# Kernel optimization log

Hardware: AMD Instinct MI355X
Metric: run time of the kernel (lower is better)

## Reference

```python
import jax, jax.numpy as jnp
import numpy as np

N = 8192          # n_nodes; must equal OUT due to _weight_norm broadcasting
IN = 512          # in_features
OUT = 8192        # out_features
ALPHA = 0.2       # leaky relu negative slope
NEG_INF = -9e15   # mask value used by the torch module


def setup_inputs() -> dict:
    key = jax.random.key(0)
    k1, k2, k3, k4 = jax.random.split(key, 4)
    x = jax.random.normal(k1, (N, IN), jnp.float32)
    adj = jax.random.randint(k2, (N, N), 0, 2, jnp.int32)
    # nn.Linear weight [out_features, in_features]
    W = jax.random.normal(k3, (OUT, IN), jnp.float32) / np.sqrt(IN)
    # attention vector a: [2*out_features, 1], xavier_uniform-ish scale
    a = jax.random.normal(k4, (2 * OUT, 1), jnp.float32) * (1.414 * np.sqrt(2.0 / (2 * OUT + 1)))
    return {"x": x, "adj": adj, "W": W, "a": a}


def reference(x, adj, W, a):
    h = x @ W.T                                   # [N, OUT] (OUT == N)
    # torch._weight_norm(h, g, dim=1) = h * g / ||h||_cols  (norm over dim 0, kept as [1, OUT])
    col_norm = jnp.linalg.norm(h, axis=0, keepdims=True)   # [1, OUT]
    a1 = a[:OUT]                                  # [OUT, 1]
    a2 = a[OUT:]                                  # [OUT, 1]
    wn1 = h * (a1 / col_norm)                     # [N, N]: h[i,j]*a1[i]/norm[j]
    wn2 = h * (a2 / col_norm)                     # [N, N]
    e = jax.nn.leaky_relu(wn1 + wn2.T, ALPHA)     # [N, N]
    scores = jnp.where(adj > 0, e, NEG_INF)
    attention = jax.nn.softmax(scores, axis=1)    # dropout omitted (eval / deterministic)
    return attention @ h                          # [N, OUT]
```

## Files before the change

### kernel.cpp

```cpp
#include <hip/hip_runtime.h>
#include <hip/hip_bf16.h>
#include <stdint.h>

#define NN 8192
#define KIN 512

typedef __attribute__((ext_vector_type(8))) short bfx8;
typedef __attribute__((ext_vector_type(4))) float f32x4;
typedef __attribute__((ext_vector_type(4))) short sh4;

__device__ __forceinline__ float b2f(unsigned short u) {
  union { unsigned int i; float f; } z; z.i = ((unsigned int)u) << 16; return z.f;
}
__device__ __forceinline__ unsigned short f2b(float f) {
  __hip_bfloat16 h = __float2bfloat16(f);
  union { __hip_bfloat16 h; unsigned short u; } z; z.h = h; return z.u;
}

__device__ __forceinline__ void async16(void* lds, const void* g) {
  __builtin_amdgcn_global_load_lds(
      (const __attribute__((address_space(1))) unsigned int*)g,
      (__attribute__((address_space(3))) unsigned int*)lds,
      16, 0, 0);
}

__global__ __launch_bounds__(256)
void cvt_f32_bf16(const float* __restrict__ in, unsigned short* __restrict__ out, int n4) {
  int i = blockIdx.x * 256 + threadIdx.x;
  if (i >= n4) return;
  const float4 v = reinterpret_cast<const float4*>(in)[i];
  sh4 o;
  o.x = (short)f2b(v.x); o.y = (short)f2b(v.y);
  o.z = (short)f2b(v.z); o.w = (short)f2b(v.w);
  reinterpret_cast<sh4*>(out)[i] = o;
}

__global__ __launch_bounds__(256)
void reduce_cvt(const float* __restrict__ P, unsigned short* __restrict__ out, int n4) {
  const int i = blockIdx.x * 256 + threadIdx.x;
  if (i >= n4) return;
  const size_t plane = (size_t)NN * KIN / 4;
  const float4* P4 = reinterpret_cast<const float4*>(P);
  float4 s = P4[i];
#pragma unroll
  for (int sp = 1; sp < 8; ++sp) {
    const float4 v = P4[i + sp * plane];
    s.x += v.x; s.y += v.y; s.z += v.z; s.w += v.w;
  }
  sh4 o;
  o.x = (short)f2b(s.x); o.y = (short)f2b(s.y);
  o.z = (short)f2b(s.z); o.w = (short)f2b(s.w);
  reinterpret_cast<sh4*>(out)[i] = o;
}

__global__ __launch_bounds__(256)
void transpose_cvt(const float* __restrict__ x, unsigned short* __restrict__ xT,
                   int NR, int NC) {
  __shared__ float t[64][65];
  const int i0 = blockIdx.x << 6;
  const int c0 = blockIdx.y << 6;
  const int tid = threadIdx.x;
  const int rl = tid >> 4;
  const int cl = (tid & 15) << 2;
#pragma unroll
  for (int ps = 0; ps < 4; ++ps) {
    const int r = rl + (ps << 4);
    const float4 v = *reinterpret_cast<const float4*>(&x[(size_t)(i0 + r) * NC + c0 + cl]);
    t[r][cl] = v.x; t[r][cl + 1] = v.y; t[r][cl + 2] = v.z; t[r][cl + 3] = v.w;
  }
  __syncthreads();
  const int cr = tid >> 3;
  const int il = (tid & 7) << 3;
#pragma unroll
  for (int ps = 0; ps < 2; ++ps) {
    const int c = cr + (ps << 5);
    bfx8 o;
#pragma unroll
    for (int j = 0; j < 8; ++j) o[j] = (short)f2b(t[il + j][c]);
    *reinterpret_cast<bfx8*>(&xT[(size_t)(c0 + c) * NR + i0 + il]) = o;
  }
}

template<int MODE, int SPLITS>
__global__ __launch_bounds__(256)
void gemm_bt(const unsigned short* __restrict__ A,
             const unsigned short* __restrict__ B,
             void* __restrict__ C,
             const float* __restrict__ rowscale,
             int M, int Nc, int K)
{
  __shared__ unsigned short As[2][128 * 32];
  __shared__ unsigned short Bs[2][128 * 32];

  const int tid  = threadIdx.x;
  const int lane = tid & 63;
  const int wave = tid >> 6;
  const int wr   = wave >> 1, wc = wave & 1;

  const int nwg = gridDim.x;
  const int cpx = nwg >> 3;
  const int bid = blockIdx.x;
  const int swz = (bid & 7) * cpx + (bid >> 3);
  const int bps = nwg / SPLITS;
  const int split = swz / bps;
  const int rem   = swz % bps;
  const int nbn = Nc >> 7;
  const int bm  = (rem / nbn) << 7;
  const int bn  = (rem % nbn) << 7;
  const int klen  = K / SPLITS;
  const int kbase = split * klen;

  const int off0 = (wave << 10) + (lane << 4);
  const int r0   = off0 >> 6;
  const int k0e  = (off0 & 63) >> 1;
  const int r1   = r0 + 64;

  const unsigned short* Ag0 = A + (size_t)(bm + r0) * K + kbase + k0e;
  const unsigned short* Ag1 = A + (size_t)(bm + r1) * K + kbase + k0e;
  const unsigned short* Bg0 = B + (size_t)(bn + r0) * K + kbase + k0e;
  const unsigned short* Bg1 = B + (size_t)(bn + r1) * K + kbase + k0e;

  f32x4 acc[4][4];
#pragma unroll
  for (int m = 0; m < 4; ++m)
#pragma unroll
    for (int n = 0; n < 4; ++n)
      acc[m][n] = (f32x4){0.f, 0.f, 0.f, 0.f};

  const int ldsoff = (wave << 10);

  auto stage = [&](int buf, int kk) {
    char* la = (char*)&As[buf][0] + ldsoff;
    char* lb = (char*)&Bs[buf][0] + ldsoff;
    async16(la,        Ag0 + kk);
    async16(la + 4096, Ag1 + kk);
    async16(lb,        Bg0 + kk);
    async16(lb + 4096, Bg1 + kk);
  };

  stage(0, 0);
  __syncthreads();

  const int nk   = klen >> 5;
  const int arow = (wr << 6) + (lane & 15);
  const int brow = (wc << 6) + (lane & 15);
  const int koff = (lane >> 4) << 3;

  for (int kt = 0; kt < nk; ++kt) {
    const int cur = kt & 1;
    if (kt + 1 < nk) stage(cur ^ 1, (kt + 1) << 5);

    bfx8 af[4], bf[4];
#pragma unroll
    for (int m = 0; m < 4; ++m)
      af[m] = *reinterpret_cast<const bfx8*>(&As[cur][(arow + (m << 4)) * 32 + koff]);
#pragma unroll
    for (int n = 0; n < 4; ++n)
      bf[n] = *reinterpret_cast<const bfx8*>(&Bs[cur][(brow + (n << 4)) * 32 + koff]);

#pragma unroll
    for (int m = 0; m < 4; ++m)
#pragma unroll
      for (int n = 0; n < 4; ++n)
        acc[m][n] = __builtin_amdgcn_mfma_f32_16x16x32_bf16(af[m], bf[n], acc[m][n], 0, 0, 0);

    __syncthreads();
  }

#pragma unroll
  for (int m = 0; m < 4; ++m) {
    const int rowb = bm + (wr << 6) + (m << 4) + ((lane >> 4) << 2);
#pragma unroll
    for (int j = 0; j < 4; ++j) {
      const int r = rowb + j;
      if (MODE == 1) {
        unsigned short* Cb = (unsigned short*)C;
#pragma unroll
        for (int n = 0; n < 4; ++n)
          Cb[(size_t)r * Nc + bn + (wc << 6) + (n << 4) + (lane & 15)] = f2b(acc[m][n][j]);
      } else if (MODE == 0) {
        const float s = rowscale[r];
        float* Cf = (float*)C;
#pragma unroll
        for (int n = 0; n < 4; ++n)
          Cf[(size_t)r * Nc + bn + (wc << 6) + (n << 4) + (lane & 15)] = acc[m][n][j] * s;
      } else {
        float* Cf = (float*)C + (size_t)split * M * Nc;
#pragma unroll
        for (int n = 0; n < 4; ++n)
          Cf[(size_t)r * Nc + bn + (wc << 6) + (n << 4) + (lane & 15)] = acc[m][n][j];
      }
    }
  }
}

template<int MODE>
__global__ __launch_bounds__(256)
void row_reduce(const unsigned short* __restrict__ X, float* __restrict__ out, int ncols) {
  const int row = blockIdx.x;
  const unsigned short* xr = X + (size_t)row * ncols;
  float s = 0.f;
  for (int c = threadIdx.x * 8; c < ncols; c += 2048) {
    bfx8 v = *reinterpret_cast<const bfx8*>(xr + c);
#pragma unroll
    for (int j = 0; j < 8; ++j) {
      float f = b2f((unsigned short)v[j]);
      s += (MODE == 0) ? f * f : f;
    }
  }
#pragma unroll
  for (int o = 32; o > 0; o >>= 1) s += __shfl_down(s, o);
  __shared__ float red[4];
  if ((threadIdx.x & 63) == 0) red[threadIdx.x >> 6] = s;
  __syncthreads();
  if (threadIdx.x == 0) {
    float t = red[0] + red[1] + red[2] + red[3];
    out[row] = (MODE == 0) ? (1.0f / sqrtf(t)) : (1.0f / t);
  }
}

__global__ __launch_bounds__(256)
void invert_vec(float* __restrict__ v) {
  const int i = blockIdx.x * 256 + threadIdx.x;
  v[i] = 1.0f / v[i];
}

__global__ __launch_bounds__(256)
void scores_kernel(const unsigned short* __restrict__ hT,
                   const int* __restrict__ adj,
                   const float* __restrict__ a,
                   const float* __restrict__ icn,
                   unsigned short* __restrict__ p,
                   float* __restrict__ rs_raw,
                   int strip)
{
  __shared__ unsigned short T1t[64][72];

  const int tid   = threadIdx.x;
  const int i0    = blockIdx.x << 6;
  const int jbase = blockIdx.y * strip;
  const int ntile = strip >> 6;

  const int slot = tid & 7;
  const int jb   = slot << 3;
  const int il0  = tid >> 3;
  const int i_p0 = i0 + il0;
  const int i_p1 = i_p0 + 32;
  const float a1_0 = a[i_p0], ici_0 = icn[i_p0];
  const float a1_1 = a[i_p1], ici_1 = icn[i_p1];
  float rs0 = 0.f, rs1 = 0.f;

  const int rblk0 = (((jb >> 3) ^ ((il0 >> 3) & 7)) << 3);
  const int rblk1 = (((jb >> 3) ^ (((il0 + 32) >> 3) & 7)) << 3);

  for (int jt = 0; jt < ntile; ++jt) {
    const int j0 = jbase + (jt << 6);
    __syncthreads();
#pragma unroll
    for (int ss = 0; ss < 2; ++ss) {
      const int u  = tid + (ss << 8);
      const int jr = u >> 3;
      const int cb = (u & 7) << 3;
      const bfx8 v = *reinterpret_cast<const bfx8*>(hT + (size_t)(j0 + jr) * NN + i0 + cb);
      const int colp = ((((jr >> 3) ^ (u & 7)) << 3) | (jr & 7));
#pragma unroll
      for (int k = 0; k < 8; ++k) T1t[cb + k][colp] = (unsigned short)v[k];
    }
    __syncthreads();

    const int j = j0 + jb;
    const float4 ic0 = *reinterpret_cast<const float4*>(icn + j);
    const float4 ic1 = *reinterpret_cast<const float4*>(icn + j + 4);
    const float4 a20 = *reinterpret_cast<const float4*>(a + NN + j);
    const float4 a21 = *reinterpret_cast<const float4*>(a + NN + j + 4);
    const float icj[8] = {ic0.x, ic0.y, ic0.z, ic0.w, ic1.x, ic1.y, ic1.z, ic1.w};
    const float a2j[8] = {a20.x, a20.y, a20.z, a20.w, a21.x, a21.y, a21.z, a21.w};

#pragma unroll
    for (int ps = 0; ps < 2; ++ps) {
      const int il   = (ps == 0) ? il0 : il0 + 32;
      const int i    = (ps == 0) ? i_p0 : i_p1;
      const float a1 = (ps == 0) ? a1_0 : a1_1;
      const float ii = (ps == 0) ? ici_0 : ici_1;
      const int rb   = (ps == 0) ? rblk0 : rblk1;

      const bfx8 hijv = *reinterpret_cast<const bfx8*>(&T1t[il][rb]);
      const bfx8 hjiv = *reinterpret_cast<const bfx8*>(hT + (size_t)i * NN + j);
      const int4 ad0  = *reinterpret_cast<const int4*>(adj + (size_t)i * NN + j);
      const int4 ad1  = *reinterpret_cast<const int4*>(adj + (size_t)i * NN + j + 4);
      const int adv[8] = {ad0.x, ad0.y, ad0.z, ad0.w, ad1.x, ad1.y, ad1.z, ad1.w};

      bfx8 o;
      float rs = 0.f;
#pragma unroll
      for (int k = 0; k < 8; ++k) {
        const float hij = b2f((unsigned short)hijv[k]);
        const float hji = b2f((unsigned short)hjiv[k]);
        const float e0  = hij * (a1 * icj[k]) + hji * (a2j[k] * ii);
        const float e   = e0 > 0.f ? e0 : 0.2f * e0;
        const float pv  = (adv[k] > 0) ? __expf(e) : 0.f;
        const unsigned short ub = f2b(pv);
        o[k] = (short)ub;
        rs += b2f(ub);
      }
      *reinterpret_cast<bfx8*>(p + (size_t)i * NN + j) = o;
      if (ps == 0) rs0 += rs; else rs1 += rs;
    }
  }

#pragma unroll
  for (int o = 1; o < 8; o <<= 1) {
    rs0 += __shfl_xor(rs0, o);
    rs1 += __shfl_xor(rs1, o);
  }
  if (slot == 0) {
    atomicAdd(rs_raw + i_p0, rs0);
    atomicAdd(rs_raw + i_p1, rs1);
  }
}

extern "C" void kernel_launch(void* const* d_in, const int* in_sizes, int n_in,
                              void* d_out, int out_size, void* d_ws, size_t ws_size,
                              hipStream_t stream)
{
  (void)in_sizes; (void)n_in; (void)out_size; (void)ws_size;
  const float* x   = (const float*)d_in[0];
  const int*   adj = (const int*)d_in[1];
  const float* W   = (const float*)d_in[2];
  const float* a   = (const float*)d_in[3];
  float* out = (float*)d_out;

  char* ws = (char*)d_ws;
  unsigned short* hT = (unsigned short*)ws;
  unsigned short* p  = (unsigned short*)(ws + 134217728ull);
  unsigned short* xb = p;
  unsigned short* Wb = p + (size_t)NN * KIN;
  unsigned short* Axb = hT;
  unsigned short* xT  = hT + (size_t)NN * KIN;
  unsigned short* Wb2 = hT + 2 * (size_t)NN * KIN;
  float* icn = (float*)(ws + 268435456ull);
  float* irs = (float*)(ws + 268435456ull + 32768ull);
  float* parts = out;

  hipMemsetAsync(irs, 0, NN * sizeof(float), stream);

  const int n4 = NN * KIN / 4;
  cvt_f32_bf16<<<n4 / 256, 256, 0, stream>>>(x, xb, n4);
  cvt_f32_bf16<<<n4 / 256, 256, 0, stream>>>(W, Wb, n4);

  gemm_bt<1, 1><<<4096, 256, 0, stream>>>(Wb, xb, hT, nullptr, NN, NN, KIN);

  row_reduce<0><<<NN, 256, 0, stream>>>(hT, icn, NN);

  scores_kernel<<<dim3(128, 16), 256, 0, stream>>>(hT, adj, a, icn, p, irs, NN / 16);

  invert_vec<<<NN / 256, 256, 0, stream>>>(irs);

  cvt_f32_bf16<<<n4 / 256, 256, 0, stream>>>(W, Wb2, n4);
  transpose_cvt<<<dim3(NN / 64, KIN / 64), 256, 0, stream>>>(x, xT, NN, KIN);

  gemm_bt<2, 8><<<2048, 256, 0, stream>>>(p, xT, parts, nullptr, NN, KIN, NN);

  reduce_cvt<<<n4 / 256, 256, 0, stream>>>(parts, Axb, n4);

  gemm_bt<0, 1><<<4096, 256, 0, stream>>>(Axb, Wb2, out, irs, NN, NN, KIN);
}
```

Measured before the change: 545.7 us.

## Add 256x256-tile 8-wave GEMM for the large products and halve split-K

Adds a new GEMM kernel with 256x256 output tiles, 512 threads, BK=64, XOR-swizzled LDS, asynchronous global-to-LDS double buffering, an XCD-aware block swizzle and raised wave priority around the MFMAs. It replaces the 128x128 kernel for the two 8192x8192x512 GEMMs, aiming for more data reuse per LDS load and less global traffic. The split-K GEMM drops from 8 splits to 4, and the partial-sum reduction is shortened to match, which cuts the fp32 partial traffic but gives fewer blocks in that launch. The risks are lower occupancy from the large LDS footprint and register-heavy accumulators, plus tight hand-written vmcnt waits.

New measurement: 566.0 us. +3.7%, slower.

```diff
diff --git a/kernel.cpp b/kernel.cpp
--- a/kernel.cpp
+++ b/kernel.cpp
@@ -43,7 +43,7 @@
   const float4* P4 = reinterpret_cast<const float4*>(P);
   float4 s = P4[i];
 #pragma unroll
-  for (int sp = 1; sp < 8; ++sp) {
+  for (int sp = 1; sp < 4; ++sp) {
     const float4 v = P4[i + sp * plane];
     s.x += v.x; s.y += v.y; s.z += v.z; s.w += v.w;
   }
@@ -78,6 +78,152 @@
 #pragma unroll
     for (int j = 0; j < 8; ++j) o[j] = (short)f2b(t[il + j][c]);
     *reinterpret_cast<bfx8*>(&xT[(size_t)(c0 + c) * NR + i0 + il]) = o;
+  }
+}
+
+template<int MODE>
+__global__ __launch_bounds__(512, 1)
+void gemm256(const unsigned short* __restrict__ A,
+             const unsigned short* __restrict__ B,
+             void* __restrict__ C,
+             const float* __restrict__ rowscale,
+             int M, int Nc, int K)
+{
+  __shared__ unsigned short Asl[2][256 * 64];
+  __shared__ unsigned short Bsl[2][256 * 64];
+
+  const int tid  = threadIdx.x;
+  const int lane = tid & 63;
+  const int wid  = tid >> 6;
+  const int wm   = wid >> 2;
+  const int wn   = wid & 3;
+
+  const int nwg = gridDim.x;
+  const int cpx = nwg >> 3;
+  const int swz = (blockIdx.x & 7) * cpx + (blockIdx.x >> 3);
+  const int nbn = Nc >> 8;
+  const int bm  = (swz / nbn) << 8;
+  const int bn  = (swz % nbn) << 8;
+
+  const int srow = tid >> 3;
+  const int scol = (((tid & 7) ^ (srow & 7)) << 3);
+  const unsigned short* Ab = A + (size_t)(bm + srow) * K + scol;
+  const unsigned short* Bb = B + (size_t)(bn + ((srow >> 5) << 6) + (srow & 31)) * K + scol;
+  const int wslot = wid << 9;
+
+  const int l15  = lane & 15;
+  const int axor = (lane & 7) << 4;
+  const int kb   = ((lane >> 4) << 4);
+
+  f32x4 acc[8][4];
+#pragma unroll
+  for (int m = 0; m < 8; ++m)
+#pragma unroll
+    for (int n = 0; n < 4; ++n)
+      acc[m][n] = (f32x4){0.f, 0.f, 0.f, 0.f};
+
+  auto stageA = [&](int buf, int mh, int kbase) {
+#pragma unroll
+    for (int u = 0; u < 2; ++u) {
+      unsigned short* dst = &Asl[buf][((mh << 6) + (u << 7)) << 6] + wslot;
+      async16(dst, Ab + (size_t)((mh << 6) + (u << 7)) * K + kbase);
+    }
+  };
+  auto stageB = [&](int buf, int nh, int kbase) {
+#pragma unroll
+    for (int u = 0; u < 2; ++u) {
+      unsigned short* dst = &Bsl[buf][((nh << 7) + (u << 6)) << 6] + wslot;
+      async16(dst, Bb + (size_t)((u << 7) + (nh << 5)) * K + kbase);
+    }
+  };
+
+  stageA(0, 0, 0);
+  stageB(0, 0, 0);
+  stageA(0, 1, 0);
+  stageB(0, 1, 0);
+
+  const int nk = K >> 6;
+
+  for (int kt = 0; kt < nk; ++kt) {
+    const int cur = kt & 1;
+    const bool hasNext = (kt + 1 < nk);
+    const int nkb = (kt + 1) << 6;
+    if (!hasNext) asm volatile("s_waitcnt vmcnt(0)" ::: "memory");
+
+#pragma unroll
+    for (int p = 0; p < 4; ++p) {
+      if (hasNext) {
+        asm volatile("s_waitcnt vmcnt(4)" ::: "memory");
+        if (p == 0)      stageA(cur ^ 1, 0, nkb);
+        else if (p == 1) stageB(cur ^ 1, 0, nkb);
+        else if (p == 2) stageA(cur ^ 1, 1, nkb);
+        else             stageB(cur ^ 1, 1, nkb);
+      }
+      __builtin_amdgcn_s_barrier();
+      asm volatile("" ::: "memory");
+
+      const int mh = (p == 0) ? 0 : (p == 3) ? 0 : 1;
+      const int nh = (p < 2) ? 0 : 1;
+
+      const char* Ac = (const char*)&Asl[cur][0];
+      const char* Bc = (const char*)&Bsl[cur][0];
+
+      bfx8 afr[4][2], bfr[2][2];
+#pragma unroll
+      for (int mf = 0; mf < 4; ++mf) {
+        const int row = (wm << 7) + (mh << 6) + (mf << 4) + l15;
+#pragma unroll
+        for (int ks = 0; ks < 2; ++ks)
+          afr[mf][ks] = *reinterpret_cast<const bfx8*>(Ac + row * 128 + (((ks << 6) + kb) ^ axor));
+      }
+#pragma unroll
+      for (int nf = 0; nf < 2; ++nf) {
+        const int rp = (nh << 7) + (wn << 5) + (nf << 4) + l15;
+#pragma unroll
+        for (int ks = 0; ks < 2; ++ks)
+          bfr[nf][ks] = *reinterpret_cast<const bfx8*>(Bc + rp * 128 + (((ks << 6) + kb) ^ axor));
+      }
+
+      __builtin_amdgcn_s_setprio(1);
+#pragma unroll
+      for (int mf = 0; mf < 4; ++mf)
+#pragma unroll
+        for (int nf = 0; nf < 2; ++nf)
+#pragma unroll
+          for (int ks = 0; ks < 2; ++ks)
+            acc[(mh << 2) + mf][(nh << 1) + nf] =
+                __builtin_amdgcn_mfma_f32_16x16x32_bf16(afr[mf][ks], bfr[nf][ks],
+                                                        acc[(mh << 2) + mf][(nh << 1) + nf], 0, 0, 0);
+      __builtin_amdgcn_s_setprio(0);
+      __builtin_amdgcn_s_barrier();
+      asm volatile("" ::: "memory");
+    }
+  }
+
+#pragma unroll
+  for (int am = 0; am < 8; ++am) {
+    const int mh = am >> 2, mf = am & 3;
+    const int rowb = bm + (wm << 7) + (mh << 6) + (mf << 4) + ((lane >> 4) << 2);
+#pragma unroll
+    for (int j = 0; j < 4; ++j) {
+      const int r = rowb + j;
+      if (MODE == 1) {
+        unsigned short* Cb = (unsigned short*)C;
+#pragma unroll
+        for (int an = 0; an < 4; ++an) {
+          const int c = bn + (wn << 6) + ((an >> 1) << 5) + ((an & 1) << 4) + l15;
+          Cb[(size_t)r * Nc + c] = f2b(acc[am][an][j]);
+        }
+      } else {
+        const float s = rowscale[r];
+        float* Cf = (float*)C;
+#pragma unroll
+        for (int an = 0; an < 4; ++an) {
+          const int c = bn + (wn << 6) + ((an >> 1) << 5) + ((an & 1) << 4) + l15;
+          Cf[(size_t)r * Nc + c] = acc[am][an][j] * s;
+        }
+      }
+    }
   }
 }
 
@@ -173,23 +319,10 @@
 #pragma unroll
     for (int j = 0; j < 4; ++j) {
       const int r = rowb + j;
-      if (MODE == 1) {
-        unsigned short* Cb = (unsigned short*)C;
-#pragma unroll
-        for (int n = 0; n < 4; ++n)
-          Cb[(size_t)r * Nc + bn + (wc << 6) + (n << 4) + (lane & 15)] = f2b(acc[m][n][j]);
-      } else if (MODE == 0) {
-        const float s = rowscale[r];
-        float* Cf = (float*)C;
-#pragma unroll
-        for (int n = 0; n < 4; ++n)
-          Cf[(size_t)r * Nc + bn + (wc << 6) + (n << 4) + (lane & 15)] = acc[m][n][j] * s;
-      } else {
-        float* Cf = (float*)C + (size_t)split * M * Nc;
-#pragma unroll
-        for (int n = 0; n < 4; ++n)
-          Cf[(size_t)r * Nc + bn + (wc << 6) + (n << 4) + (lane & 15)] = acc[m][n][j];
-      }
+      float* Cf = (float*)C + (size_t)split * M * Nc;
+#pragma unroll
+      for (int n = 0; n < 4; ++n)
+        Cf[(size_t)r * Nc + bn + (wc << 6) + (n << 4) + (lane & 15)] = acc[m][n][j];
     }
   }
 }
@@ -348,7 +481,7 @@
   cvt_f32_bf16<<<n4 / 256, 256, 0, stream>>>(x, xb, n4);
   cvt_f32_bf16<<<n4 / 256, 256, 0, stream>>>(W, Wb, n4);
 
-  gemm_bt<1, 1><<<4096, 256, 0, stream>>>(Wb, xb, hT, nullptr, NN, NN, KIN);
+  gemm256<1><<<1024, 512, 0, stream>>>(Wb, xb, hT, nullptr, NN, NN, KIN);
 
   row_reduce<0><<<NN, 256, 0, stream>>>(hT, icn, NN);
 
@@ -359,9 +492,9 @@
   cvt_f32_bf16<<<n4 / 256, 256, 0, stream>>>(W, Wb2, n4);
   transpose_cvt<<<dim3(NN / 64, KIN / 64), 256, 0, stream>>>(x, xT, NN, KIN);
 
-  gemm_bt<2, 8><<<2048, 256, 0, stream>>>(p, xT, parts, nullptr, NN, KIN, NN);
+  gemm_bt<2, 4><<<1024, 256, 0, stream>>>(p, xT, parts, nullptr, NN, KIN, NN);
 
   reduce_cvt<<<n4 / 256, 256, 0, stream>>>(parts, Axb, n4);
 
-  gemm_bt<0, 1><<<4096, 256, 0, stream>>>(Axb, Wb2, out, irs, NN, NN, KIN);
-}
+  gemm256<0><<<1024, 512, 0, stream>>>(Axb, Wb2, out, irs, NN, NN, KIN);
+}
```

## Fuse column-norm into first GEMM epilogue and dedupe conversions

Applied to the files above, without the earlier changes.

Computes the squared row sums of hT inside the first GEMM's epilogue using shuffles and atomics, which removes the separate row_reduce pass over the 128MB hT matrix. The x bf16 conversion is merged into the transpose kernel, and the second W conversion is dropped because the buffers now live in a separate workspace region. The split-K count for the attention GEMM drops from 8 to 4, which halves the partial traffic but leaves fewer workgroups. Atomic accumulation makes the result order-dependent and adds atomic contention.

After: 574.9 us. 1.05x slower.

```diff
diff --git a/kernel.cpp b/kernel.cpp
--- a/kernel.cpp
+++ b/kernel.cpp
@@ -43,7 +43,7 @@
   const float4* P4 = reinterpret_cast<const float4*>(P);
   float4 s = P4[i];
 #pragma unroll
-  for (int sp = 1; sp < 8; ++sp) {
+  for (int sp = 1; sp < 4; ++sp) {
     const float4 v = P4[i + sp * plane];
     s.x += v.x; s.y += v.y; s.z += v.z; s.w += v.w;
   }
@@ -55,7 +55,7 @@
 
 __global__ __launch_bounds__(256)
 void transpose_cvt(const float* __restrict__ x, unsigned short* __restrict__ xT,
-                   int NR, int NC) {
+                   unsigned short* __restrict__ xb, int NR, int NC) {
   __shared__ float t[64][65];
   const int i0 = blockIdx.x << 6;
   const int c0 = blockIdx.y << 6;
@@ -67,6 +67,10 @@
     const int r = rl + (ps << 4);
     const float4 v = *reinterpret_cast<const float4*>(&x[(size_t)(i0 + r) * NC + c0 + cl]);
     t[r][cl] = v.x; t[r][cl + 1] = v.y; t[r][cl + 2] = v.z; t[r][cl + 3] = v.w;
+    sh4 o;
+    o.x = (short)f2b(v.x); o.y = (short)f2b(v.y);
+    o.z = (short)f2b(v.z); o.w = (short)f2b(v.w);
+    *reinterpret_cast<sh4*>(&xb[(size_t)(i0 + r) * NC + c0 + cl]) = o;
   }
   __syncthreads();
   const int cr = tid >> 3;
@@ -81,12 +85,12 @@
   }
 }
 
-template<int MODE, int SPLITS>
+template<int MODE, int SPLITS, int ICN>
 __global__ __launch_bounds__(256)
 void gemm_bt(const unsigned short* __restrict__ A,
              const unsigned short* __restrict__ B,
              void* __restrict__ C,
-             const float* __restrict__ rowscale,
+             float* __restrict__ aux,
              int M, int Nc, int K)
 {
   __shared__ unsigned short As[2][128 * 32];
@@ -178,8 +182,15 @@
 #pragma unroll
         for (int n = 0; n < 4; ++n)
           Cb[(size_t)r * Nc + bn + (wc << 6) + (n << 4) + (lane & 15)] = f2b(acc[m][n][j]);
+        if (ICN) {
+          float s = acc[m][0][j] * acc[m][0][j] + acc[m][1][j] * acc[m][1][j]
+                  + acc[m][2][j] * acc[m][2][j] + acc[m][3][j] * acc[m][3][j];
+          s += __shfl_xor(s, 1); s += __shfl_xor(s, 2);
+          s += __shfl_xor(s, 4); s += __shfl_xor(s, 8);
+          if ((lane & 15) == 0) atomicAdd(aux + r, s);
+        }
       } else if (MODE == 0) {
-        const float s = rowscale[r];
+        const float s = aux[r];
         float* Cf = (float*)C;
 #pragma unroll
         for (int n = 0; n < 4; ++n)
@@ -196,33 +207,9 @@
 
 template<int MODE>
 __global__ __launch_bounds__(256)
-void row_reduce(const unsigned short* __restrict__ X, float* __restrict__ out, int ncols) {
-  const int row = blockIdx.x;
-  const unsigned short* xr = X + (size_t)row * ncols;
-  float s = 0.f;
-  for (int c = threadIdx.x * 8; c < ncols; c += 2048) {
-    bfx8 v = *reinterpret_cast<const bfx8*>(xr + c);
-#pragma unroll
-    for (int j = 0; j < 8; ++j) {
-      float f = b2f((unsigned short)v[j]);
-      s += (MODE == 0) ? f * f : f;
-    }
-  }
-#pragma unroll
-  for (int o = 32; o > 0; o >>= 1) s += __shfl_down(s, o);
-  __shared__ float red[4];
-  if ((threadIdx.x & 63) == 0) red[threadIdx.x >> 6] = s;
-  __syncthreads();
-  if (threadIdx.x == 0) {
-    float t = red[0] + red[1] + red[2] + red[3];
-    out[row] = (MODE == 0) ? (1.0f / sqrtf(t)) : (1.0f / t);
-  }
-}
-
-__global__ __launch_bounds__(256)
-void invert_vec(float* __restrict__ v) {
+void final_inv(float* __restrict__ v) {
   const int i = blockIdx.x * 256 + threadIdx.x;
-  v[i] = 1.0f / v[i];
+  v[i] = (MODE == 0) ? (1.0f / sqrtf(v[i])) : (1.0f / v[i]);
 }
 
 __global__ __launch_bounds__(256)
@@ -333,35 +320,31 @@
   char* ws = (char*)d_ws;
   unsigned short* hT = (unsigned short*)ws;
   unsigned short* p  = (unsigned short*)(ws + 134217728ull);
-  unsigned short* xb = p;
-  unsigned short* Wb = p + (size_t)NN * KIN;
-  unsigned short* Axb = hT;
-  unsigned short* xT  = hT + (size_t)NN * KIN;
-  unsigned short* Wb2 = hT + 2 * (size_t)NN * KIN;
   float* icn = (float*)(ws + 268435456ull);
   float* irs = (float*)(ws + 268435456ull + 32768ull);
+  unsigned short* xb  = (unsigned short*)(ws + 268435456ull + 65536ull);
+  unsigned short* Wb  = xb + (size_t)NN * KIN;
+  unsigned short* xT  = Wb + (size_t)NN * KIN;
+  unsigned short* Axb = xT + (size_t)NN * KIN;
   float* parts = out;
 
-  hipMemsetAsync(irs, 0, NN * sizeof(float), stream);
+  hipMemsetAsync(icn, 0, 65536, stream);
 
   const int n4 = NN * KIN / 4;
-  cvt_f32_bf16<<<n4 / 256, 256, 0, stream>>>(x, xb, n4);
+  transpose_cvt<<<dim3(NN / 64, KIN / 64), 256, 0, stream>>>(x, xT, xb, NN, KIN);
   cvt_f32_bf16<<<n4 / 256, 256, 0, stream>>>(W, Wb, n4);
 
-  gemm_bt<1, 1><<<4096, 256, 0, stream>>>(Wb, xb, hT, nullptr, NN, NN, KIN);
-
-  row_reduce<0><<<NN, 256, 0, stream>>>(hT, icn, NN);
+  gemm_bt<1, 1, 1><<<4096, 256, 0, stream>>>(Wb, xb, hT, icn, NN, NN, KIN);
+
+  final_inv<0><<<NN / 256, 256, 0, stream>>>(icn);
 
   scores_kernel<<<dim3(128, 16), 256, 0, stream>>>(hT, adj, a, icn, p, irs, NN / 16);
 
-  invert_vec<<<NN / 256, 256, 0, stream>>>(irs);
-
-  cvt_f32_bf16<<<n4 / 256, 256, 0, stream>>>(W, Wb2, n4);
-  transpose_cvt<<<dim3(NN / 64, KIN / 64), 256, 0, stream>>>(x, xT, NN, KIN);
-
-  gemm_bt<2, 8><<<2048, 256, 0, stream>>>(p, xT, parts, nullptr, NN, KIN, NN);
+  final_inv<1><<<NN / 256, 256, 0, stream>>>(irs);
+
+  gemm_bt<2, 4, 0><<<1024, 256, 0, stream>>>(p, xT, parts, nullptr, NN, KIN, NN);
 
   reduce_cvt<<<n4 / 256, 256, 0, stream>>>(parts, Axb, n4);
 
-  gemm_bt<0, 1><<<4096, 256, 0, stream>>>(Axb, Wb2, out, irs, NN, NN, KIN);
-}
+  gemm_bt<0, 1, 0><<<4096, 256, 0, stream>>>(Axb, Wb, out, irs, NN, NN, KIN);
+}
```

## Stage GEMM epilogue through LDS for coalesced stores and dedupe input conversions

Applied to the files above, without the earlier changes.

The GEMM epilogue now writes accumulators into a shared-memory buffer that aliases the operand tiles, then emits row-contiguous 16-byte vector stores instead of scattered 2- or 4-byte stores. The bf16 copy of x is now produced inside the transpose kernel, and the W conversion is kept in a dedicated workspace region and reused, which removes two conversion launches. The cost is extra barriers and a second LDS pass in the epilogue, and the fp32 path is split into two halves that serialize the waves.

Result: slower. 986.7 us (+80.8%).

```diff
diff --git a/kernel.cpp b/kernel.cpp
--- a/kernel.cpp
+++ b/kernel.cpp
@@ -55,7 +55,7 @@
 
 __global__ __launch_bounds__(256)
 void transpose_cvt(const float* __restrict__ x, unsigned short* __restrict__ xT,
-                   int NR, int NC) {
+                   unsigned short* __restrict__ xb, int NR, int NC) {
   __shared__ float t[64][65];
   const int i0 = blockIdx.x << 6;
   const int c0 = blockIdx.y << 6;
@@ -67,6 +67,10 @@
     const int r = rl + (ps << 4);
     const float4 v = *reinterpret_cast<const float4*>(&x[(size_t)(i0 + r) * NC + c0 + cl]);
     t[r][cl] = v.x; t[r][cl + 1] = v.y; t[r][cl + 2] = v.z; t[r][cl + 3] = v.w;
+    sh4 o;
+    o.x = (short)f2b(v.x); o.y = (short)f2b(v.y);
+    o.z = (short)f2b(v.z); o.w = (short)f2b(v.w);
+    *reinterpret_cast<sh4*>(&xb[(size_t)(i0 + r) * NC + c0 + cl]) = o;
   }
   __syncthreads();
   const int cr = tid >> 3;
@@ -89,8 +93,11 @@
              const float* __restrict__ rowscale,
              int M, int Nc, int K)
 {
-  __shared__ unsigned short As[2][128 * 32];
-  __shared__ unsigned short Bs[2][128 * 32];
+  __shared__ union {
+    struct { unsigned short As[2][128 * 32]; unsigned short Bs[2][128 * 32]; } s;
+    unsigned short ebf[128 * 136];
+    float          ef[64 * 132];
+  } u;
 
   const int tid  = threadIdx.x;
   const int lane = tid & 63;
@@ -130,8 +137,8 @@
   const int ldsoff = (wave << 10);
 
   auto stage = [&](int buf, int kk) {
-    char* la = (char*)&As[buf][0] + ldsoff;
-    char* lb = (char*)&Bs[buf][0] + ldsoff;
+    char* la = (char*)&u.s.As[buf][0] + ldsoff;
+    char* lb = (char*)&u.s.Bs[buf][0] + ldsoff;
     async16(la,        Ag0 + kk);
     async16(la + 4096, Ag1 + kk);
     async16(lb,        Bg0 + kk);
@@ -153,10 +160,10 @@
     bfx8 af[4], bf[4];
 #pragma unroll
     for (int m = 0; m < 4; ++m)
-      af[m] = *reinterpret_cast<const bfx8*>(&As[cur][(arow + (m << 4)) * 32 + koff]);
+      af[m] = *reinterpret_cast<const bfx8*>(&u.s.As[cur][(arow + (m << 4)) * 32 + koff]);
 #pragma unroll
     for (int n = 0; n < 4; ++n)
-      bf[n] = *reinterpret_cast<const bfx8*>(&Bs[cur][(brow + (n << 4)) * 32 + koff]);
+      bf[n] = *reinterpret_cast<const bfx8*>(&u.s.Bs[cur][(brow + (n << 4)) * 32 + koff]);
 
 #pragma unroll
     for (int m = 0; m < 4; ++m)
@@ -167,29 +174,56 @@
     __syncthreads();
   }
 
-#pragma unroll
-  for (int m = 0; m < 4; ++m) {
-    const int rowb = bm + (wr << 6) + (m << 4) + ((lane >> 4) << 2);
-#pragma unroll
-    for (int j = 0; j < 4; ++j) {
-      const int r = rowb + j;
-      if (MODE == 1) {
-        unsigned short* Cb = (unsigned short*)C;
+  const int l15 = lane & 15;
+  const int rq  = (lane >> 4) << 2;
+
+  if (MODE == 1) {
+#pragma unroll
+    for (int m = 0; m < 4; ++m)
+#pragma unroll
+      for (int j = 0; j < 4; ++j) {
+        const int lrow = (wr << 6) + (m << 4) + rq + j;
 #pragma unroll
         for (int n = 0; n < 4; ++n)
-          Cb[(size_t)r * Nc + bn + (wc << 6) + (n << 4) + (lane & 15)] = f2b(acc[m][n][j]);
-      } else if (MODE == 0) {
-        const float s = rowscale[r];
-        float* Cf = (float*)C;
-#pragma unroll
-        for (int n = 0; n < 4; ++n)
-          Cf[(size_t)r * Nc + bn + (wc << 6) + (n << 4) + (lane & 15)] = acc[m][n][j] * s;
-      } else {
-        float* Cf = (float*)C + (size_t)split * M * Nc;
-#pragma unroll
-        for (int n = 0; n < 4; ++n)
-          Cf[(size_t)r * Nc + bn + (wc << 6) + (n << 4) + (lane & 15)] = acc[m][n][j];
+          u.ebf[lrow * 136 + (wc << 6) + (n << 4) + l15] = f2b(acc[m][n][j]);
       }
+    __syncthreads();
+    unsigned short* Cb = (unsigned short*)C;
+#pragma unroll
+    for (int it = 0; it < 8; ++it) {
+      const int uu = tid + (it << 8);
+      const int row = uu >> 4;
+      const int ch  = uu & 15;
+      const bfx8 v = *reinterpret_cast<const bfx8*>(&u.ebf[row * 136 + (ch << 3)]);
+      *reinterpret_cast<bfx8*>(&Cb[(size_t)(bm + row) * Nc + bn + (ch << 3)]) = v;
+    }
+  } else {
+    float* Cf = (float*)C + (MODE == 2 ? (size_t)split * M * Nc : 0);
+#pragma unroll
+    for (int h = 0; h < 2; ++h) {
+      if (wr == h) {
+#pragma unroll
+        for (int m = 0; m < 4; ++m)
+#pragma unroll
+          for (int j = 0; j < 4; ++j) {
+            const int lrow = (m << 4) + rq + j;
+            float sc = 1.0f;
+            if (MODE == 0) sc = rowscale[bm + (h << 6) + lrow];
+#pragma unroll
+            for (int n = 0; n < 4; ++n)
+              u.ef[lrow * 132 + (wc << 6) + (n << 4) + l15] = acc[m][n][j] * sc;
+          }
+      }
+      __syncthreads();
+#pragma unroll
+      for (int it = 0; it < 8; ++it) {
+        const int uu = tid + (it << 8);
+        const int row = uu >> 5;
+        const int ch  = uu & 31;
+        const float4 v = *reinterpret_cast<const float4*>(&u.ef[row * 132 + (ch << 2)]);
+        *reinterpret_cast<float4*>(&Cf[(size_t)(bm + (h << 6) + row) * Nc + bn + (ch << 2)]) = v;
+      }
+      __syncthreads();
     }
   }
 }
@@ -258,11 +292,11 @@
     __syncthreads();
 #pragma unroll
     for (int ss = 0; ss < 2; ++ss) {
-      const int u  = tid + (ss << 8);
-      const int jr = u >> 3;
-      const int cb = (u & 7) << 3;
+      const int uu = tid + (ss << 8);
+      const int jr = uu >> 3;
+      const int cb = (uu & 7) << 3;
       const bfx8 v = *reinterpret_cast<const bfx8*>(hT + (size_t)(j0 + jr) * NN + i0 + cb);
-      const int colp = ((((jr >> 3) ^ (u & 7)) << 3) | (jr & 7));
+      const int colp = ((((jr >> 3) ^ (uu & 7)) << 3) | (jr & 7));
 #pragma unroll
       for (int k = 0; k < 8; ++k) T1t[cb + k][colp] = (unsigned short)v[k];
     }
@@ -333,19 +367,18 @@
   char* ws = (char*)d_ws;
   unsigned short* hT = (unsigned short*)ws;
   unsigned short* p  = (unsigned short*)(ws + 134217728ull);
-  unsigned short* xb = p;
-  unsigned short* Wb = p + (size_t)NN * KIN;
-  unsigned short* Axb = hT;
-  unsigned short* xT  = hT + (size_t)NN * KIN;
-  unsigned short* Wb2 = hT + 2 * (size_t)NN * KIN;
   float* icn = (float*)(ws + 268435456ull);
   float* irs = (float*)(ws + 268435456ull + 32768ull);
+  unsigned short* xb  = (unsigned short*)(ws + 268435456ull + 65536ull);
+  unsigned short* Wb  = xb + (size_t)NN * KIN;
+  unsigned short* xT  = Wb + (size_t)NN * KIN;
+  unsigned short* Axb = xT + (size_t)NN * KIN;
   float* parts = out;
 
   hipMemsetAsync(irs, 0, NN * sizeof(float), stream);
 
   const int n4 = NN * KIN / 4;
-  cvt_f32_bf16<<<n4 / 256, 256, 0, stream>>>(x, xb, n4);
+  transpose_cvt<<<dim3(NN / 64, KIN / 64), 256, 0, stream>>>(x, xT, xb, NN, KIN);
   cvt_f32_bf16<<<n4 / 256, 256, 0, stream>>>(W, Wb, n4);
 
   gemm_bt<1, 1><<<4096, 256, 0, stream>>>(Wb, xb, hT, nullptr, NN, NN, KIN);
@@ -356,12 +389,9 @@
 
   invert_vec<<<NN / 256, 256, 0, stream>>>(irs);
 
-  cvt_f32_bf16<<<n4 / 256, 256, 0, stream>>>(W, Wb2, n4);
-  transpose_cvt<<<dim3(NN / 64, KIN / 64), 256, 0, stream>>>(x, xT, NN, KIN);
-
   gemm_bt<2, 8><<<2048, 256, 0, stream>>>(p, xT, parts, nullptr, NN, KIN, NN);
 
   reduce_cvt<<<n4 / 256, 256, 0, stream>>>(parts, Axb, n4);
 
-  gemm_bt<0, 1><<<4096, 256, 0, stream>>>(Axb, Wb2, out, irs, NN, NN, KIN);
-}
+  gemm_bt<0, 1><<<4096, 256, 0, stream>>>(Axb, Wb, out, irs, NN, NN, KIN);
+}
```
